# Kernel optimization log

Hardware: AMD Instinct MI355X
Metric: run time of the kernel (lower is better)

The kernel has to match this reference:

```python
import jax, jax.numpy as jnp
import numpy as np

B, S, H, I = 2, 2048, 4096, 16384
EPS = 1e-12


def setup_inputs() -> dict:
    key = jax.random.key(0)
    ks = jax.random.split(key, 8)
    w_scale = 0.02
    return {
        "input": jax.random.normal(ks[0], (B, S, H), jnp.float32),
        "residual": jax.random.normal(ks[1], (B, S, H), jnp.float32),
        "bias": jax.random.normal(ks[2], (H,), jnp.float32) * w_scale,
        "attn_nw": jnp.ones((H,), jnp.float32),
        "attn_nb": jnp.zeros((H,), jnp.float32),
        "inter_w": jax.random.normal(ks[3], (I, H), jnp.float32) * w_scale,
        "inter_b": jax.random.normal(ks[4], (I,), jnp.float32) * w_scale,
        "output_w": jax.random.normal(ks[5], (H, I), jnp.float32) * w_scale,
        "output_b": jax.random.normal(ks[6], (H,), jnp.float32) * w_scale,
    }


def reference(input, residual, bias, attn_nw, attn_nb, inter_w, inter_b, output_w, output_b):
    # Fused mlp_gemm: residual_add = input + residual + attn-output bias
    residual_add = input + residual + bias  # [B,S,H]
    # LayerNorm over hidden dim with attn_nw/attn_nb
    mean = jnp.mean(residual_add, axis=-1, keepdims=True)
    var = jnp.var(residual_add, axis=-1, keepdims=True)
    ln = (residual_add - mean) * jax.lax.rsqrt(var + EPS) * attn_nw + attn_nb
    # Intermediate GEMM + bias + GELU (DeepSpeed uses tanh-approx gelu)
    inter = jax.nn.gelu(jnp.einsum("bsh,ih->bsi", ln, inter_w) + inter_b, approximate=True)
    # Output projection (vector_matmul)
    out = jnp.einsum("bsi,hi->bsh", inter, output_w)
    # bias_residual: add residual_add and output bias
    return out + residual_add + output_b
```

## Files before the change

kernel.cpp:

```cpp
#include <hip/hip_runtime.h>
#include <hip/hip_bf16.h>
#include <cstdint>
#include <math.h>

typedef __attribute__((ext_vector_type(4))) float f32x4;
typedef __attribute__((ext_vector_type(8))) __bf16 bf16x8;

__device__ __forceinline__ unsigned short f2bf(float f) {
    union { float f; unsigned u; } v; v.f = f;
    unsigned u = v.u + 0x7fffu + ((v.u >> 16) & 1u);
    return (unsigned short)(u >> 16);
}

__device__ __forceinline__ float gelu_tanh(float x) {
    float x3 = x * x * x;
    float t = tanhf(0.7978845608028654f * (x + 0.044715f * x3));
    return 0.5f * x * (1.0f + t);
}

__device__ __forceinline__ void gload_lds16(const void* g, void* l) {
    __builtin_amdgcn_global_load_lds(
        (__attribute__((address_space(1))) void*)(uintptr_t)g,
        (__attribute__((address_space(3))) void*)(unsigned)(uintptr_t)l,
        16, 0, 0);
}

__global__ __launch_bounds__(256)
void fused_add_ln(const float* __restrict__ in, const float* __restrict__ res,
                  const float* __restrict__ bias, const float* __restrict__ nw,
                  const float* __restrict__ nb, float* __restrict__ resadd,
                  unsigned short* __restrict__ lnout, int H) {
    const int row = blockIdx.x;
    const int tid = threadIdx.x;
    const size_t base = (size_t)row * H;
    float v[16];
    float s = 0.f, ss = 0.f;
#pragma unroll
    for (int i = 0; i < 4; ++i) {
        int idx = (i * 256 + tid) * 4;
        float4 a = *(const float4*)(in + base + idx);
        float4 b = *(const float4*)(res + base + idx);
        float4 c = *(const float4*)(bias + idx);
        float x0 = a.x + b.x + c.x, x1 = a.y + b.y + c.y;
        float x2 = a.z + b.z + c.z, x3 = a.w + b.w + c.w;
        v[i * 4 + 0] = x0; v[i * 4 + 1] = x1; v[i * 4 + 2] = x2; v[i * 4 + 3] = x3;
        s += x0 + x1 + x2 + x3;
        ss += x0 * x0 + x1 * x1 + x2 * x2 + x3 * x3;
    }
#pragma unroll
    for (int off = 32; off > 0; off >>= 1) {
        s += __shfl_down(s, off);
        ss += __shfl_down(ss, off);
    }
    __shared__ float red[8];
    const int w = tid >> 6;
    if ((tid & 63) == 0) { red[w] = s; red[4 + w] = ss; }
    __syncthreads();
    s = red[0] + red[1] + red[2] + red[3];
    ss = red[4] + red[5] + red[6] + red[7];
    const float mean = s / H;
    const float var = ss / H - mean * mean;
    const float rstd = rsqrtf(var + 1e-12f);
#pragma unroll
    for (int i = 0; i < 4; ++i) {
        int idx = (i * 256 + tid) * 4;
        float4 wv = *(const float4*)(nw + idx);
        float4 bv = *(const float4*)(nb + idx);
        float4 r;
        r.x = v[i * 4 + 0]; r.y = v[i * 4 + 1]; r.z = v[i * 4 + 2]; r.w = v[i * 4 + 3];
        *(float4*)(resadd + base + idx) = r;
        ushort4 o;
        o.x = f2bf((r.x - mean) * rstd * wv.x + bv.x);
        o.y = f2bf((r.y - mean) * rstd * wv.y + bv.y);
        o.z = f2bf((r.z - mean) * rstd * wv.z + bv.z);
        o.w = f2bf((r.w - mean) * rstd * wv.w + bv.w);
        *(ushort4*)(lnout + base + idx) = o;
    }
}

__global__ __launch_bounds__(256)
void cast_w(const float* __restrict__ w, unsigned short* __restrict__ o, long long n4) {
    long long i = (long long)blockIdx.x * 256 + threadIdx.x;
    if (i >= n4) return;
    float4 f = *(const float4*)(w + i * 4);
    ushort4 u;
    u.x = f2bf(f.x); u.y = f2bf(f.y); u.z = f2bf(f.z); u.w = f2bf(f.w);
    *(ushort4*)(o + i * 4) = u;
}

#define GBM 256
#define GBN 256

#define STAGE(s, mat, h, T) do {                                              \
    const unsigned short* _src = ((mat) ? pB : pA)                            \
        + (size_t)((h) * 128) * K + (size_t)(T) * 64;                         \
    char* _dst = ldsc + (s) * 65536 + (mat) * 32768 + (h) * 16384 + dOff;     \
    gload_lds16(_src, _dst);                                                  \
    gload_lds16(_src + (size_t)64 * K, _dst + 8192);                          \
} while (0)

#define RD_B(s) do {                                                          \
    _Pragma("unroll")                                                         \
    for (int ni = 0; ni < 4; ++ni)                                            \
        _Pragma("unroll")                                                     \
        for (int kk = 0; kk < 2; ++kk)                                        \
            bq[ni][kk] = *(const bf16x8*)(ldsc + (s) * 65536 + 32768          \
                + ((wc * 64 + ni * 16 + lrow) << 7) + ckk[kk]);               \
} while (0)

#define RD_A(q, s) do {                                                       \
    _Pragma("unroll")                                                         \
    for (int m2 = 0; m2 < 2; ++m2)                                            \
        _Pragma("unroll")                                                     \
        for (int kk = 0; kk < 2; ++kk)                                        \
            aq[m2][kk] = *(const bf16x8*)(ldsc + (s) * 65536                  \
                + ((wr * 128 + ((q) * 2 + m2) * 16 + lrow) << 7) + ckk[kk]);  \
} while (0)

#define MF(q) do {                                                            \
    __builtin_amdgcn_s_setprio(1);                                            \
    _Pragma("unroll")                                                         \
    for (int kk = 0; kk < 2; ++kk)                                            \
        _Pragma("unroll")                                                     \
        for (int m2 = 0; m2 < 2; ++m2)                                        \
            _Pragma("unroll")                                                 \
            for (int ni = 0; ni < 4; ++ni)                                    \
                acc[(q) * 2 + m2][ni] = __builtin_amdgcn_mfma_f32_16x16x32_bf16( \
                    aq[m2][kk], bq[ni][kk], acc[(q) * 2 + m2][ni], 0, 0, 0);  \
    __builtin_amdgcn_s_setprio(0);                                            \
} while (0)

#define LG do { asm volatile("s_waitcnt lgkmcnt(0)" ::: "memory");            \
                __builtin_amdgcn_sched_barrier(0); } while (0)
#define BAR   asm volatile("s_barrier" ::: "memory")
#define GATE2 asm volatile("s_waitcnt vmcnt(2)" ::: "memory")
#define GATE4 asm volatile("s_waitcnt vmcnt(4)" ::: "memory")
#define GATE0 asm volatile("s_waitcnt vmcnt(0)" ::: "memory")

template <int EPI>
__global__ __launch_bounds__(512, 2)
void gemm256(const unsigned short* __restrict__ A,
             const unsigned short* __restrict__ B,
             const float* __restrict__ bias_n,
             const float* __restrict__ resadd,
             void* __restrict__ Cout,
             int M, int N, int K) {
    __shared__ unsigned short lds[2][2][2][128 * 64];
    char* ldsc = (char*)&lds[0][0][0][0];
    const int tid = threadIdx.x;
    const int lane = tid & 63;
    const int w = tid >> 6;
    const int wr = w >> 2;
    const int wc = w & 3;

    const int nwg = gridDim.x;
    const int lg = (blockIdx.x & 7) * (nwg >> 3) + (blockIdx.x >> 3);
    const int nbx = N / GBN;
    const int brow = lg / nbx;
    const int bcol = lg % nbx;

    const int srow = tid >> 3;
    const int scol = ((((tid & 7) << 4) ^ ((srow & 7) << 4)) >> 1);
    const unsigned short* pA = A + (size_t)(brow * GBM + srow) * K + scol;
    const unsigned short* pB = B + (size_t)(bcol * GBN + srow) * K + scol;
    const int dOff = tid * 16;

    const int lrow = lane & 15;
    int ckk[2];
    ckk[0] = (((lane >> 4) << 4)) ^ ((lrow & 7) << 4);
    ckk[1] = ckk[0] ^ 64;

    f32x4 acc[8][4] = {};
    bf16x8 aq[2][2];
    bf16x8 bq[4][2];

    const int NT = K / 64;
    const int niter = NT / 2;

    STAGE(0, 1, 0, 0); STAGE(0, 1, 1, 0);
    STAGE(0, 0, 0, 0); STAGE(0, 0, 1, 0);
    STAGE(1, 1, 0, 1); STAGE(1, 1, 1, 1);
    GATE4;
    BAR;
    RD_B(0);

    for (int i = 0; i < niter - 1; ++i) {
        const int T1 = 2 * i + 1, T2 = 2 * i + 2, T3 = 2 * i + 3;
        RD_A(0, 0);                 BAR; STAGE(1, 0, 0, T1); LG; MF(0);
        RD_A(1, 0);                 BAR; STAGE(1, 0, 1, T1); LG; MF(1);
        RD_A(2, 0);                 BAR; STAGE(0, 1, 0, T2); LG; MF(2);
        RD_A(3, 0); GATE2;          BAR; STAGE(0, 1, 1, T2); LG; MF(3); RD_B(1);
        RD_A(0, 1);                 BAR; STAGE(0, 0, 0, T2); LG; MF(0);
        RD_A(1, 1);                 BAR; STAGE(0, 0, 1, T2); LG; MF(1);
        RD_A(2, 1);                 BAR; STAGE(1, 1, 0, T3); LG; MF(2);
        RD_A(3, 1); GATE2;          BAR; STAGE(1, 1, 1, T3); LG; MF(3); RD_B(0);
    }
    {
        const int T1 = NT - 1;
        RD_A(0, 0);                 BAR; STAGE(1, 0, 0, T1); LG; MF(0);
        RD_A(1, 0);                 BAR; STAGE(1, 0, 1, T1); LG; MF(1);
        RD_A(2, 0);                 BAR;                     LG; MF(2);
        RD_A(3, 0); GATE0;          BAR;                     LG; MF(3); RD_B(1);
        RD_A(0, 1);                 BAR;                     LG; MF(0);
        RD_A(1, 1);                 BAR;                     LG; MF(1);
        RD_A(2, 1);                 BAR;                     LG; MF(2);
        RD_A(3, 1);                 BAR;                     LG; MF(3);
    }

    const int c0 = bcol * GBN + wc * 64 + lrow;
    const int r0 = brow * GBM + wr * 128 + (lane >> 4) * 4;
#pragma unroll
    for (int mi = 0; mi < 8; ++mi) {
#pragma unroll
        for (int j = 0; j < 4; ++j) {
            const int row = r0 + mi * 16 + j;
#pragma unroll
            for (int ni = 0; ni < 4; ++ni) {
                const int col = c0 + ni * 16;
                float x = acc[mi][ni][j] + bias_n[col];
                if (EPI == 0) {
                    ((unsigned short*)Cout)[(size_t)row * N + col] = f2bf(gelu_tanh(x));
                } else {
                    const size_t off = (size_t)row * N + col;
                    ((float*)Cout)[off] = x + resadd[off];
                }
            }
        }
    }
}

extern "C" void kernel_launch(void* const* d_in, const int* in_sizes, int n_in,
                              void* d_out, int out_size, void* d_ws, size_t ws_size,
                              hipStream_t stream) {
    const float* input    = (const float*)d_in[0];
    const float* residual = (const float*)d_in[1];
    const float* bias     = (const float*)d_in[2];
    const float* attn_nw  = (const float*)d_in[3];
    const float* attn_nb  = (const float*)d_in[4];
    const float* inter_w  = (const float*)d_in[5];
    const float* inter_b  = (const float*)d_in[6];
    const float* output_w = (const float*)d_in[7];
    const float* output_b = (const float*)d_in[8];

    const int H = in_sizes[3];
    const int I = in_sizes[6];
    const int T = in_sizes[0] / H;

    char* ws = (char*)d_ws;
    float* resadd      = (float*)ws;
    unsigned short* ln = (unsigned short*)(ws + (size_t)T * H * 4);
    unsigned short* w1 = (unsigned short*)((char*)ln + (size_t)T * H * 2);
    unsigned short* w2 = w1 + (size_t)I * H;
    unsigned short* act = w2 + (size_t)H * I;

    fused_add_ln<<<T, 256, 0, stream>>>(input, residual, bias, attn_nw, attn_nb,
                                        resadd, ln, H);

    {
        long long n4 = (long long)I * H / 4;
        int blocks = (int)((n4 + 255) / 256);
        cast_w<<<blocks, 256, 0, stream>>>(inter_w, w1, n4);
        cast_w<<<blocks, 256, 0, stream>>>(output_w, w2, n4);
    }

    {
        dim3 grid((T / GBM) * (I / GBN));
        gemm256<0><<<grid, 512, 0, stream>>>(ln, w1, inter_b, nullptr, act, T, I, H);
    }

    {
        dim3 grid((T / GBM) * (H / GBN));
        gemm256<1><<<grid, 512, 0, stream>>>(act, w2, output_b, resadd, d_out, T, H, I);
    }
}
```

Measured before the change: 1.099 ms.

## Halve barrier count by processing two A sub-tiles per pipeline phase

Restructures the GEMM main loop from eight phases per iteration to four. Each phase now loads two A sub-tiles, issues both half-stages of global-to-LDS copies, and runs twice as many MFMAs between barriers. The aim is to cut barrier and waitcnt overhead and give longer MFMA bursts. In exchange it uses more registers for A fragments and full vmcnt(0) waits instead of partial waits, which may reduce load/compute overlap.

```diff
diff --git a/kernel.cpp b/kernel.cpp
--- a/kernel.cpp
+++ b/kernel.cpp
@@ -108,32 +108,38 @@
                 + ((wc * 64 + ni * 16 + lrow) << 7) + ckk[kk]);               \
 } while (0)
 
-#define RD_A(q, s) do {                                                       \
+#define RD_A2(q, s) do {                                                      \
     _Pragma("unroll")                                                         \
-    for (int m2 = 0; m2 < 2; ++m2)                                            \
+    for (int b = 0; b < 2; ++b)                                               \
         _Pragma("unroll")                                                     \
-        for (int kk = 0; kk < 2; ++kk)                                        \
-            aq[m2][kk] = *(const bf16x8*)(ldsc + (s) * 65536                  \
-                + ((wr * 128 + ((q) * 2 + m2) * 16 + lrow) << 7) + ckk[kk]);  \
-} while (0)
-
-#define MF(q) do {                                                            \
+        for (int m2 = 0; m2 < 2; ++m2)                                        \
+            _Pragma("unroll")                                                 \
+            for (int kk = 0; kk < 2; ++kk)                                    \
+                aq[b][m2][kk] = *(const bf16x8*)(ldsc + (s) * 65536           \
+                    + ((wr * 128 + (((q) + b) * 2 + m2) * 16 + lrow) << 7)    \
+                    + ckk[kk]);                                               \
+} while (0)
+
+#define MF2(q) do {                                                          \
     __builtin_amdgcn_s_setprio(1);                                            \
     _Pragma("unroll")                                                         \
     for (int kk = 0; kk < 2; ++kk)                                            \
         _Pragma("unroll")                                                     \
-        for (int m2 = 0; m2 < 2; ++m2)                                        \
+        for (int b = 0; b < 2; ++b)                                           \
             _Pragma("unroll")                                                 \
-            for (int ni = 0; ni < 4; ++ni)                                    \
-                acc[(q) * 2 + m2][ni] = __builtin_amdgcn_mfma_f32_16x16x32_bf16( \
-                    aq[m2][kk], bq[ni][kk], acc[(q) * 2 + m2][ni], 0, 0, 0);  \
+            for (int m2 = 0; m2 < 2; ++m2)                                    \
+                _Pragma("unroll")                                             \
+                for (int ni = 0; ni < 4; ++ni)                                \
+                    acc[((q) + b) * 2 + m2][ni] =                             \
+                        __builtin_amdgcn_mfma_f32_16x16x32_bf16(              \
+                            aq[b][m2][kk], bq[ni][kk],                        \
+                            acc[((q) + b) * 2 + m2][ni], 0, 0, 0);            \
     __builtin_amdgcn_s_setprio(0);                                            \
 } while (0)
 
 #define LG do { asm volatile("s_waitcnt lgkmcnt(0)" ::: "memory");            \
                 __builtin_amdgcn_sched_barrier(0); } while (0)
 #define BAR   asm volatile("s_barrier" ::: "memory")
-#define GATE2 asm volatile("s_waitcnt vmcnt(2)" ::: "memory")
 #define GATE4 asm volatile("s_waitcnt vmcnt(4)" ::: "memory")
 #define GATE0 asm volatile("s_waitcnt vmcnt(0)" ::: "memory")
 
@@ -171,7 +177,7 @@
     ckk[1] = ckk[0] ^ 64;
 
     f32x4 acc[8][4] = {};
-    bf16x8 aq[2][2];
+    bf16x8 aq[2][2][2];
     bf16x8 bq[4][2];
 
     const int NT = K / 64;
@@ -186,25 +192,25 @@
 
     for (int i = 0; i < niter - 1; ++i) {
         const int T1 = 2 * i + 1, T2 = 2 * i + 2, T3 = 2 * i + 3;
-        RD_A(0, 0);                 BAR; STAGE(1, 0, 0, T1); LG; MF(0);
-        RD_A(1, 0);                 BAR; STAGE(1, 0, 1, T1); LG; MF(1);
-        RD_A(2, 0);                 BAR; STAGE(0, 1, 0, T2); LG; MF(2);
-        RD_A(3, 0); GATE2;          BAR; STAGE(0, 1, 1, T2); LG; MF(3); RD_B(1);
-        RD_A(0, 1);                 BAR; STAGE(0, 0, 0, T2); LG; MF(0);
-        RD_A(1, 1);                 BAR; STAGE(0, 0, 1, T2); LG; MF(1);
-        RD_A(2, 1);                 BAR; STAGE(1, 1, 0, T3); LG; MF(2);
-        RD_A(3, 1); GATE2;          BAR; STAGE(1, 1, 1, T3); LG; MF(3); RD_B(0);
+        RD_A2(0, 0);         BAR;
+        STAGE(1, 0, 0, T1); STAGE(1, 0, 1, T1); LG; MF2(0);
+        RD_A2(2, 0); GATE0;  BAR;
+        STAGE(0, 1, 0, T2); STAGE(0, 1, 1, T2); LG; MF2(2); RD_B(1);
+        RD_A2(0, 1);         BAR;
+        STAGE(0, 0, 0, T2); STAGE(0, 0, 1, T2); LG; MF2(0);
+        RD_A2(2, 1); GATE0;  BAR;
+        STAGE(1, 1, 0, T3); STAGE(1, 1, 1, T3); LG; MF2(2); RD_B(0);
     }
     {
         const int T1 = NT - 1;
-        RD_A(0, 0);                 BAR; STAGE(1, 0, 0, T1); LG; MF(0);
-        RD_A(1, 0);                 BAR; STAGE(1, 0, 1, T1); LG; MF(1);
-        RD_A(2, 0);                 BAR;                     LG; MF(2);
-        RD_A(3, 0); GATE0;          BAR;                     LG; MF(3); RD_B(1);
-        RD_A(0, 1);                 BAR;                     LG; MF(0);
-        RD_A(1, 1);                 BAR;                     LG; MF(1);
-        RD_A(2, 1);                 BAR;                     LG; MF(2);
-        RD_A(3, 1);                 BAR;                     LG; MF(3);
+        RD_A2(0, 0);         BAR;
+        STAGE(1, 0, 0, T1); STAGE(1, 0, 1, T1); LG; MF2(0);
+        RD_A2(2, 0); GATE0;  BAR;
+        LG; MF2(2); RD_B(1);
+        RD_A2(0, 1);         BAR;
+        LG; MF2(0);
+        RD_A2(2, 1);         BAR;
+        LG; MF2(2);
     }
 
     const int c0 = bcol * GBN + wc * 64 + lrow;
```

New measurement: 1.344 ms. 1.22x slower.

## Restructure GEMM main-loop schedule with split barriers and partial lgkm waits

Applied to the files above, without the earlier changes.

Reorders the 8-phase main loop so B fragments load at the start of each half-iteration alongside A reads and the next-tile staging. Adds a second barrier after each MFMA block and a partial lgkmcnt(8) wait. Global-load gating moves from vmcnt(2) to vmcnt(4). The aim is to overlap LDS reads and global-to-LDS staging with MFMA work in a ping-pong style, at the cost of twice as many barriers per phase and tighter ordering assumptions on LDS buffer reuse.

```diff
diff --git a/kernel.cpp b/kernel.cpp
--- a/kernel.cpp
+++ b/kernel.cpp
@@ -132,8 +132,8 @@
 
 #define LG do { asm volatile("s_waitcnt lgkmcnt(0)" ::: "memory");            \
                 __builtin_amdgcn_sched_barrier(0); } while (0)
+#define LGK8  asm volatile("s_waitcnt lgkmcnt(8)" ::: "memory")
 #define BAR   asm volatile("s_barrier" ::: "memory")
-#define GATE2 asm volatile("s_waitcnt vmcnt(2)" ::: "memory")
 #define GATE4 asm volatile("s_waitcnt vmcnt(4)" ::: "memory")
 #define GATE0 asm volatile("s_waitcnt vmcnt(0)" ::: "memory")
 
@@ -182,29 +182,28 @@
     STAGE(1, 1, 0, 1); STAGE(1, 1, 1, 1);
     GATE4;
     BAR;
-    RD_B(0);
 
     for (int i = 0; i < niter - 1; ++i) {
         const int T1 = 2 * i + 1, T2 = 2 * i + 2, T3 = 2 * i + 3;
-        RD_A(0, 0);                 BAR; STAGE(1, 0, 0, T1); LG; MF(0);
-        RD_A(1, 0);                 BAR; STAGE(1, 0, 1, T1); LG; MF(1);
-        RD_A(2, 0);                 BAR; STAGE(0, 1, 0, T2); LG; MF(2);
-        RD_A(3, 0); GATE2;          BAR; STAGE(0, 1, 1, T2); LG; MF(3); RD_B(1);
-        RD_A(0, 1);                 BAR; STAGE(0, 0, 0, T2); LG; MF(0);
-        RD_A(1, 1);                 BAR; STAGE(0, 0, 1, T2); LG; MF(1);
-        RD_A(2, 1);                 BAR; STAGE(1, 1, 0, T3); LG; MF(2);
-        RD_A(3, 1); GATE2;          BAR; STAGE(1, 1, 1, T3); LG; MF(3); RD_B(0);
+        RD_B(0); RD_A(0, 0); STAGE(1, 0, 0, T1); LGK8;  BAR; LG; MF(0); BAR;
+        RD_A(1, 0);          STAGE(1, 0, 1, T1);        BAR; LG; MF(1); BAR;
+        RD_A(2, 0);          STAGE(0, 1, 0, T2);        BAR; LG; MF(2); BAR;
+        RD_A(3, 0);          STAGE(0, 1, 1, T2); GATE4; BAR; LG; MF(3); BAR;
+        RD_B(1); RD_A(0, 1); STAGE(0, 0, 0, T2); LGK8;  BAR; LG; MF(0); BAR;
+        RD_A(1, 1);          STAGE(0, 0, 1, T2);        BAR; LG; MF(1); BAR;
+        RD_A(2, 1);          STAGE(1, 1, 0, T3);        BAR; LG; MF(2); BAR;
+        RD_A(3, 1);          STAGE(1, 1, 1, T3); GATE4; BAR; LG; MF(3); BAR;
     }
     {
         const int T1 = NT - 1;
-        RD_A(0, 0);                 BAR; STAGE(1, 0, 0, T1); LG; MF(0);
-        RD_A(1, 0);                 BAR; STAGE(1, 0, 1, T1); LG; MF(1);
-        RD_A(2, 0);                 BAR;                     LG; MF(2);
-        RD_A(3, 0); GATE0;          BAR;                     LG; MF(3); RD_B(1);
-        RD_A(0, 1);                 BAR;                     LG; MF(0);
-        RD_A(1, 1);                 BAR;                     LG; MF(1);
-        RD_A(2, 1);                 BAR;                     LG; MF(2);
-        RD_A(3, 1);                 BAR;                     LG; MF(3);
+        RD_B(0); RD_A(0, 0); STAGE(1, 0, 0, T1); LGK8;  BAR; LG; MF(0); BAR;
+        RD_A(1, 0);          STAGE(1, 0, 1, T1);        BAR; LG; MF(1); BAR;
+        RD_A(2, 0);                                     BAR; LG; MF(2); BAR;
+        RD_A(3, 0);                              GATE0; BAR; LG; MF(3); BAR;
+        RD_B(1); RD_A(0, 1); LGK8;                      BAR; LG; MF(0); BAR;
+        RD_A(1, 1);                                     BAR; LG; MF(1); BAR;
+        RD_A(2, 1);                                     BAR; LG; MF(2); BAR;
+        RD_A(3, 1);                                     BAR; LG; MF(3);
     }
 
     const int c0 = bcol * GBN + wc * 64 + lrow;
```

Measured after the change: 1.121 ms. 2.0% more time.
